# Performance work log

Measured on AMD Instinct MI355X. Metric: run time of the kernel, lower is better.

The kernel has to match this reference:

```python
import jax, jax.numpy as jnp
import numpy as np

B, S, E, H, L, F = 64, 256, 480, 6, 8, 1920
D = E // H  # 80
VOCAB, MEL, CHORD = 4833, 257, 4833 - 257
EPS = 1e-5


def setup_inputs() -> dict:
    key = jax.random.key(0)
    ks = jax.random.split(key, 24)
    mel = jax.random.randint(ks[0], (B, S), 0, MEL)
    chd = MEL + jax.random.randint(ks[1], (B, S), 0, CHORD)
    pos = jnp.arange(S) % 2  # 0=melody, 1=chord
    input_tokens = jnp.where(pos[None, :] == 1, chd, mel)
    std = 0.02
    n = lambda k, shp: std * jax.random.normal(k, shp, dtype=jnp.float32)
    return {
        'input_tokens': input_tokens,
        'tok_emb': n(ks[2], (VOCAB, E)),
        'pos_emb': n(ks[3], (S, E)),
        'Wq': n(ks[4], (L, E, E)), 'bq': jnp.zeros((L, E)),
        'Wk': n(ks[5], (L, E, E)), 'bk': jnp.zeros((L, E)),
        'Wv': n(ks[6], (L, E, E)), 'bv': jnp.zeros((L, E)),
        'Wo': n(ks[7], (L, E, E)), 'bo': jnp.zeros((L, E)),
        'ln1_s': jnp.ones((L, E)), 'ln1_b': jnp.zeros((L, E)),
        'ln2_s': jnp.ones((L, E)), 'ln2_b': jnp.zeros((L, E)),
        'W1': n(ks[8], (L, F, E)), 'b1': jnp.zeros((L, F)),
        'W2': n(ks[9], (L, E, F)), 'b2': jnp.zeros((L, E)),
        'Wh': n(ks[10], (CHORD, E)), 'bh': jnp.zeros((CHORD,)),
    }


def _ln(x, s, b):
    mu = jnp.mean(x, -1, keepdims=True)
    var = jnp.var(x, -1, keepdims=True)
    return (x - mu) * jax.lax.rsqrt(var + EPS) * s + b


def reference(input_tokens, tok_emb, pos_emb, Wq, bq, Wk, bk, Wv, bv, Wo, bo,
              ln1_s, ln1_b, ln2_s, ln2_b, W1, b1, W2, b2, Wh, bh):
    x = tok_emb[input_tokens] + pos_emb[None, :, :]  # [B,S,E]
    causal = jnp.tril(jnp.ones((S, S), dtype=bool))  # True = keep
    scale = 1.0 / jnp.sqrt(jnp.float32(D))
    for i in range(L):
        h = _ln(x, ln1_s[i], ln1_b[i])
        q = (h @ Wq[i].T + bq[i]).reshape(B, S, H, D).transpose(0, 2, 1, 3)
        k = (h @ Wk[i].T + bk[i]).reshape(B, S, H, D).transpose(0, 2, 1, 3)
        v = (h @ Wv[i].T + bv[i]).reshape(B, S, H, D).transpose(0, 2, 1, 3)
        scores = jnp.einsum('bhsd,bhtd->bhst', q, k) * scale
        scores = jnp.where(causal[None, None], scores, -jnp.inf)
        attn = jax.nn.softmax(scores, axis=-1)
        o = jnp.einsum('bhst,bhtd->bhsd', attn, v)
        o = o.transpose(0, 2, 1, 3).reshape(B, S, E)
        x = x + (o @ Wo[i].T + bo[i])
        h2 = _ln(x, ln2_s[i], ln2_b[i])
        ff = jax.nn.gelu(h2 @ W1[i].T + b1[i], approximate=False) @ W2[i].T + b2[i]
        x = x + ff
    chord = x[:, 1::2, :]  # [B, S//2, E]
    return chord @ Wh.T + bh
```

## Files before the change

### kernel.cpp

```cpp
#include <hip/hip_runtime.h>
#include <hip/hip_bf16.h>
#include <math.h>

#define B_ 64
#define S_ 256
#define E_ 480
#define H_ 6
#define D_ 80
#define L_ 8
#define F_ 1920
#define CHORD_ 4576
#define TOKENS_ (B_*S_)
#define CROWS_ (B_*128)
#define QS_ 1440
#define KP_ 512

typedef unsigned short u16;
typedef unsigned int u32;
typedef unsigned long long u64;
typedef __attribute__((ext_vector_type(8))) short short8;
typedef __attribute__((ext_vector_type(4))) float f32x4;
typedef __attribute__((ext_vector_type(4))) u32 u32x4;

__device__ __forceinline__ u16 f2bf(float f){
  u32 u = __float_as_uint(f);
  return (u16)((u + 0x7fffu + ((u >> 16) & 1u)) >> 16);
}

__device__ __forceinline__ void async_cp16(void* lds, const void* g){
  __builtin_amdgcn_global_load_lds((const __attribute__((address_space(1))) void*)g,
                                   (__attribute__((address_space(3))) void*)lds, 16, 0, 0);
}

__device__ __forceinline__ void xcd_tile(int gx, int gy, int& tx, int& ty){
  const int nwg = gx * gy;
  const int bid = blockIdx.y * gx + blockIdx.x;
  const int xcd = bid & 7, slot = bid >> 3;
  const int q8 = nwg >> 3, r8 = nwg & 7;
  const int t = slot + (xcd < r8 ? xcd * (q8 + 1) : r8 * (q8 + 1) + (xcd - r8) * q8);
  ty = t / gx;
  tx = t - ty * gx;
}

__global__ void cvt_kernel(const float* __restrict__ s, u16* __restrict__ d, int n4)
{
  int i = blockIdx.x * 256 + threadIdx.x;
  const int stride = gridDim.x * 256;
  for (; i < n4; i += stride){
    float4 v = ((const float4*)s)[i];
    u64 w = (u64)((u32)f2bf(v.x) | ((u32)f2bf(v.y) << 16))
          | ((u64)((u32)f2bf(v.z) | ((u32)f2bf(v.w) << 16)) << 32);
    ((u64*)d)[i] = w;
  }
}

__global__ void cvt_pad_kernel(const float* __restrict__ s, u16* __restrict__ d, int nrows)
{
  const int tot = nrows * 128;
  int i = blockIdx.x * 256 + threadIdx.x;
  const int stride = gridDim.x * 256;
  for (; i < tot; i += stride){
    int row = i >> 7, c4 = i & 127;
    u64 w = 0;
    if (c4 < 120){
      float4 v = ((const float4*)(s + (size_t)row * E_))[c4];
      w = (u64)((u32)f2bf(v.x) | ((u32)f2bf(v.y) << 16))
        | ((u64)((u32)f2bf(v.z) | ((u32)f2bf(v.w) << 16)) << 32);
    }
    ((u64*)d)[i] = w;
  }
}

__global__ void qkv_cvt_kernel(const float* __restrict__ Wq, const float* __restrict__ Wk,
                               const float* __restrict__ Wv, u16* __restrict__ dst)
{
  const int tot = L_ * QS_ * 128;
  int i = blockIdx.x * 256 + threadIdx.x;
  const int stride = gridDim.x * 256;
  for (; i < tot; i += stride){
    int l = i / (QS_*128);
    int rem = i - l*(QS_*128);
    int row = rem >> 7, c4 = rem & 127;
    u64 w = 0;
    if (c4 < 120){
      const float* src = (row < 480) ? Wq + (size_t)l*E_*E_ + (size_t)row*E_
                       : (row < 960) ? Wk + (size_t)l*E_*E_ + (size_t)(row-480)*E_
                                     : Wv + (size_t)l*E_*E_ + (size_t)(row-960)*E_;
      float4 v = ((const float4*)src)[c4];
      w = (u64)((u32)f2bf(v.x) | ((u32)f2bf(v.y) << 16))
        | ((u64)((u32)f2bf(v.z) | ((u32)f2bf(v.w) << 16)) << 32);
    }
    ((u64*)dst)[i] = w;
  }
}

__global__ void bias_cat_kernel(const float* __restrict__ bq, const float* __restrict__ bk,
                                const float* __restrict__ bv, float* __restrict__ dst)
{
  int i = blockIdx.x * 256 + threadIdx.x;
  if (i >= L_*QS_) return;
  int l = i / QS_, c = i - l*QS_;
  float v = (c < 480) ? bq[l*480 + c] : (c < 960) ? bk[l*480 + c - 480] : bv[l*480 + c - 960];
  dst[i] = v;
}

__global__ void embed_kernel(const int* __restrict__ tok,
                             const float* __restrict__ tok_emb,
                             const float* __restrict__ pos_emb,
                             float* __restrict__ x)
{
  int row = blockIdx.x;
  int s = row & (S_-1);
  int t = tok[row];
  const float* te = tok_emb + (size_t)t * E_;
  const float* pe = pos_emb + (size_t)s * E_;
  float* xr = x + (size_t)row * E_;
  for (int e = threadIdx.x; e < E_; e += blockDim.x)
    xr[e] = te[e] + pe[e];
}

__global__ __launch_bounds__(256) void ln_kernel(const float* __restrict__ x,
    const float* __restrict__ g, const float* __restrict__ b, u16* __restrict__ o,
    int ldo, int pad)
{
  int wid = threadIdx.x >> 6, lane = threadIdx.x & 63;
  int row = blockIdx.x * 4 + wid;
  const float* xr = x + (size_t)row * E_;
  float v[8];
  #pragma unroll
  for (int i = 0; i < 7; ++i) v[i] = xr[lane + i*64];
  v[7] = (lane < 32) ? xr[448 + lane] : 0.f;
  float sum = 0.f, sq = 0.f;
  #pragma unroll
  for (int i = 0; i < 8; ++i){ sum += v[i]; sq += v[i]*v[i]; }
  #pragma unroll
  for (int m = 1; m < 64; m <<= 1){ sum += __shfl_xor(sum, m); sq += __shfl_xor(sq, m); }
  float mean = sum * (1.f/E_);
  float var  = sq  * (1.f/E_) - mean*mean;
  float rs = rsqrtf(var + 1e-5f);
  u16* orow = o + (size_t)row * ldo;
  #pragma unroll
  for (int i = 0; i < 7; ++i){
    int idx = lane + i*64;
    orow[idx] = f2bf((v[i]-mean)*rs*g[idx] + b[idx]);
  }
  if (lane < 32){
    int idx = 448 + lane;
    orow[idx] = f2bf((v[7]-mean)*rs*g[idx] + b[idx]);
  }
  if (pad && lane < 32) orow[480 + lane] = 0;
}

template<int MODE>
__global__ __launch_bounds__(512) void gemm_tall_kernel(const u16* __restrict__ A,
                            const u16* __restrict__ Wb, const float* __restrict__ bias,
                            u16* __restrict__ Cb, float* __restrict__ Cf,
                            int M, int N, int K, int ldc)
{
  __shared__ u16 As[2][256*32];
  __shared__ u16 Ws[2][128*32];
  const int tid = threadIdx.x;
  const int wid = tid >> 6, lane = tid & 63;
  const int wm = wid >> 1, wn = wid & 1;
  const int lr = lane & 15, kg = lane >> 4;
  const int kgs = kg ^ (lr & 3);
  int tx, ty;
  xcd_tile(gridDim.x, gridDim.y, tx, ty);
  const int m0 = ty * 256;
  const int n0 = tx * 128;

  const f32x4 zero = {0.f,0.f,0.f,0.f};
  f32x4 acc[4][4];
  #pragma unroll
  for (int i=0;i<4;i++)
    #pragma unroll
    for (int j=0;j<4;j++)
      acc[i][j] = zero;

  const int srow = tid >> 2;
  const int schunk = (tid & 3) ^ (srow & 3);
  const u16* ap0 = A + (size_t)(m0 + srow) * K + schunk*8;
  const u16* ap1 = ap0 + (size_t)128 * K;
  int r0 = n0 + srow;
  if (r0 >= N) r0 = N-1;
  const u16* wp0 = Wb + (size_t)r0 * K + schunk*8;

  #define STAGE(bb, k0) do { \
    char* ab = (char*)As[bb] + wid*1024; \
    char* wb_ = (char*)Ws[bb] + wid*1024; \
    async_cp16(ab,        ap0 + (k0)); \
    async_cp16(ab + 8192, ap1 + (k0)); \
    async_cp16(wb_,        wp0 + (k0)); \
  } while(0)

  const int nsteps = K >> 5;
  STAGE(0, 0);
  __syncthreads();
  int cur = 0;
  for (int ks = 0; ks < nsteps; ++ks){
    if (ks + 1 < nsteps) STAGE(cur^1, (ks+1) << 5);

    short8 af[4], wf[4];
    #pragma unroll
    for (int i=0;i<4;i++) af[i] = *(const short8*)&As[cur][(wm*64 + i*16 + lr)*32 + kgs*8];
    #pragma unroll
    for (int j=0;j<4;j++) wf[j] = *(const short8*)&Ws[cur][(wn*64 + j*16 + lr)*32 + kgs*8];
    #pragma unroll
    for (int i=0;i<4;i++)
      #pragma unroll
      for (int j=0;j<4;j++)
        acc[i][j] = __builtin_amdgcn_mfma_f32_16x16x32_bf16(af[i], wf[j], acc[i][j], 0, 0, 0);

    __syncthreads();
    cur ^= 1;
  }
  #undef STAGE

  #pragma unroll
  for (int i=0;i<4;i++){
    const int row = m0 + wm*64 + i*16 + kg*4;
    #pragma unroll
    for (int j=0;j<4;j++){
      const int col = n0 + wn*64 + j*16 + lr;
      if (col < N){
        const float bv = bias[col];
        #pragma unroll
        for (int q=0;q<4;q++){
          float val = acc[i][j][q] + bv;
          size_t off = (size_t)(row + q) * ldc + col;
          if (MODE == 0){
            Cb[off] = f2bf(val);
          } else if (MODE == 1){
            float gx = 0.5f * val * (1.f + erff(val * 0.70710678118654752f));
            Cb[off] = f2bf(gx);
          } else if (MODE == 2){
            Cf[off] += val;
          } else {
            Cf[off] = val;
          }
        }
      }
    }
  }
}

template<int MODE>
__global__ __launch_bounds__(256, 4) void gemm_bf_kernel(const u16* __restrict__ A,
                            const u16* __restrict__ Wb, const float* __restrict__ bias,
                            u16* __restrict__ Cb, float* __restrict__ Cf,
                            int M, int N, int K, int ldc)
{
  __shared__ u16 As[2][128*32];
  __shared__ u16 Ws[2][128*32];
  const int tid = threadIdx.x;
  const int wid = tid >> 6, lane = tid & 63;
  const int wr = wid >> 1, wc = wid & 1;
  const int lr = lane & 15, kg = lane >> 4;
  const int kgs = kg ^ (lr & 3);
  int tx, ty;
  xcd_tile(gridDim.x, gridDim.y, tx, ty);
  const int m0 = ty * 128;
  const int n0 = tx * 128;

  const f32x4 zero = {0.f,0.f,0.f,0.f};
  f32x4 acc[4][4];
  #pragma unroll
  for (int i=0;i<4;i++)
    #pragma unroll
    for (int j=0;j<4;j++)
      acc[i][j] = zero;

  const int srow = tid >> 2;
  const int schunk = (tid & 3) ^ (srow & 3);
  const u16* ap0 = A + (size_t)(m0 + srow) * K + schunk*8;
  const u16* ap1 = ap0 + (size_t)64 * K;
  int r0 = n0 + srow, r1 = r0 + 64;
  if (r0 >= N) r0 = N-1;
  if (r1 >= N) r1 = N-1;
  const u16* wp0 = Wb + (size_t)r0 * K + schunk*8;
  const u16* wp1 = Wb + (size_t)r1 * K + schunk*8;

  #define STAGE(bb, k0) do { \
    char* ab = (char*)As[bb] + wid*1024; \
    char* wb_ = (char*)Ws[bb] + wid*1024; \
    async_cp16(ab,        ap0 + (k0)); \
    async_cp16(ab + 4096, ap1 + (k0)); \
    async_cp16(wb_,        wp0 + (k0)); \
    async_cp16(wb_ + 4096, wp1 + (k0)); \
  } while(0)

  const int nsteps = K >> 5;
  STAGE(0, 0);
  __syncthreads();
  int cur = 0;
  for (int ks = 0; ks < nsteps; ++ks){
    if (ks + 1 < nsteps) STAGE(cur^1, (ks+1) << 5);

    short8 af[4], wf[4];
    #pragma unroll
    for (int i=0;i<4;i++) af[i] = *(const short8*)&As[cur][(wr*64 + i*16 + lr)*32 + kgs*8];
    #pragma unroll
    for (int j=0;j<4;j++) wf[j] = *(const short8*)&Ws[cur][(wc*64 + j*16 + lr)*32 + kgs*8];
    #pragma unroll
    for (int i=0;i<4;i++)
      #pragma unroll
      for (int j=0;j<4;j++)
        acc[i][j] = __builtin_amdgcn_mfma_f32_16x16x32_bf16(af[i], wf[j], acc[i][j], 0, 0, 0);

    __syncthreads();
    cur ^= 1;
  }
  #undef STAGE

  #pragma unroll
  for (int i=0;i<4;i++){
    const int row = m0 + wr*64 + i*16 + kg*4;
    #pragma unroll
    for (int j=0;j<4;j++){
      const int col = n0 + wc*64 + j*16 + lr;
      if (col < N){
        const float bv = bias[col];
        #pragma unroll
        for (int q=0;q<4;q++){
          float val = acc[i][j][q] + bv;
          size_t off = (size_t)(row + q) * ldc + col;
          if (MODE == 0){
            Cb[off] = f2bf(val);
          } else if (MODE == 1){
            float gx = 0.5f * val * (1.f + erff(val * 0.70710678118654752f));
            Cb[off] = f2bf(gx);
          } else if (MODE == 2){
            Cf[off] += val;
          } else {
            Cf[off] = val;
          }
        }
      }
    }
  }
}

template<int MODE>
__global__ __launch_bounds__(256) void gemm_kernel(const u16* __restrict__ A, const float* __restrict__ W,
                            const float* __restrict__ bias,
                            u16* __restrict__ Cb, float* __restrict__ Cf,
                            int M, int N, int K, int ldc)
{
  __shared__ u16 As[128*32];
  __shared__ u16 Ws[128*32];
  const int tid = threadIdx.x;
  const int wid = tid >> 6, lane = tid & 63;
  const int wr = wid >> 1, wc = wid & 1;
  const int lr = lane & 15, kg = lane >> 4;
  int tx, ty;
  xcd_tile(gridDim.x, gridDim.y, tx, ty);
  const int m0 = ty * 128;
  const int n0 = tx * 128;

  const f32x4 zero = {0.f,0.f,0.f,0.f};
  f32x4 acc[4][4];
  #pragma unroll
  for (int i=0;i<4;i++)
    #pragma unroll
    for (int j=0;j<4;j++)
      acc[i][j] = zero;

  const int trow = tid >> 1;
  const int tcol = (tid & 1) * 16;
  const int wn = n0 + trow;
  const bool wok = wn < N;
  const float* wp = W + (size_t)wn * K + tcol;

  const u16* ap0 = A + (size_t)(m0 + (tid>>2)) * K + (tid&3)*8;
  const u16* ap1 = ap0 + (size_t)64 * K;
  char* lb0 = (char*)As + wid*1024;
  char* lb1 = (char*)As + 4096 + wid*1024;
  u32* wdst = (u32*)&Ws[trow*32 + tcol];

  const int nsteps = K >> 5;
  for (int ks = 0; ks < nsteps; ++ks){
    const int k0 = ks << 5;
    async_cp16(lb0, ap0 + k0);
    async_cp16(lb1, ap1 + k0);

    float wv[16];
    if (wok){
      const float4* s4 = (const float4*)(wp + k0);
      #pragma unroll
      for (int i=0;i<4;i++){
        float4 t4 = s4[i];
        wv[4*i]=t4.x; wv[4*i+1]=t4.y; wv[4*i+2]=t4.z; wv[4*i+3]=t4.w;
      }
    } else {
      #pragma unroll
      for (int i=0;i<16;i++) wv[i]=0.f;
    }
    u32 pk[8];
    #pragma unroll
    for (int i=0;i<8;i++) pk[i] = (u32)f2bf(wv[2*i]) | ((u32)f2bf(wv[2*i+1]) << 16);
    #pragma unroll
    for (int i=0;i<8;i++) wdst[i] = pk[i];

    __syncthreads();

    short8 af[4], wf[4];
    #pragma unroll
    for (int i=0;i<4;i++) af[i] = *(const short8*)&As[(wr*64 + i*16 + lr)*32 + kg*8];
    #pragma unroll
    for (int j=0;j<4;j++) wf[j] = *(const short8*)&Ws[(wc*64 + j*16 + lr)*32 + kg*8];
    #pragma unroll
    for (int i=0;i<4;i++)
      #pragma unroll
      for (int j=0;j<4;j++)
        acc[i][j] = __builtin_amdgcn_mfma_f32_16x16x32_bf16(af[i], wf[j], acc[i][j], 0, 0, 0);

    __syncthreads();
  }

  #pragma unroll
  for (int i=0;i<4;i++){
    const int row = m0 + wr*64 + i*16 + kg*4;
    #pragma unroll
    for (int j=0;j<4;j++){
      const int col = n0 + wc*64 + j*16 + lr;
      if (col < N){
        const float bv = bias[col];
        #pragma unroll
        for (int q=0;q<4;q++){
          float val = acc[i][j][q] + bv;
          size_t off = (size_t)(row + q) * ldc + col;
          if (MODE == 0){
            Cb[off] = f2bf(val);
          } else if (MODE == 1){
            float gx = 0.5f * val * (1.f + erff(val * 0.70710678118654752f));
            Cb[off] = f2bf(gx);
          } else if (MODE == 2){
            Cf[off] += val;
          } else {
            Cf[off] = val;
          }
        }
      }
    }
  }
}

#define KSTRIDE 104
#define VSTRIDE 264
__global__ __launch_bounds__(256) void attn_mfma_kernel(const u16* __restrict__ QKV,
                                                        u16* __restrict__ O)
{
  __shared__ u16 ks[256*KSTRIDE];
  __shared__ u16 vt[80*VSTRIDE];
  const int bh = blockIdx.x;
  const int b = bh / H_, h = bh - b*H_;
  const int tid = threadIdx.x;
  const int wv = tid >> 6, lane = tid & 63;
  const int q16 = lane & 15, g = lane >> 4;
  const size_t rowbase = (size_t)(b*S_ + tid) * QS_ + h * D_;

  {
    const uint4* kr = (const uint4*)(QKV + rowbase + 480);
    uint4 t0[10];
    #pragma unroll
    for (int i=0;i<10;i++) t0[i] = kr[i];
    u16* krow = &ks[tid*KSTRIDE];
    #pragma unroll
    for (int i=0;i<10;i++) *(uint4*)&krow[i*8] = t0[i];
    const uint4 z4 = {0,0,0,0};
    *(uint4*)&krow[80] = z4;
    *(uint4*)&krow[88] = z4;
  }
  {
    const u32* vr = (const u32*)(QKV + rowbase + 960);
    u32 t1[40];
    #pragma unroll
    for (int i=0;i<40;i++) t1[i] = vr[i];
    #pragma unroll
    for (int i=0;i<40;i++){
      vt[(2*i)*VSTRIDE + tid]   = (u16)(t1[i] & 0xffffu);
      vt[(2*i+1)*VSTRIDE + tid] = (u16)(t1[i] >> 16);
    }
  }
  short8 bq[4][3];
  const short8 z8 = {0,0,0,0,0,0,0,0};
  #pragma unroll
  for (int i=0;i<4;i++){
    const int qr = 16*wv + 64*i;
    const u16* qrow = QKV + (size_t)(b*S_ + qr + q16) * QS_ + h*D_;
    bq[i][0] = *(const short8*)&qrow[g*8];
    bq[i][1] = *(const short8*)&qrow[32 + g*8];
    bq[i][2] = (g < 2) ? *(const short8*)&qrow[64 + g*8] : z8;
  }
  __syncthreads();

  f32x4 o_[4][5];
  float m_[4], l_[4];
  #pragma unroll
  for (int i=0;i<4;i++){
    m_[i] = -1e30f; l_[i] = 0.f;
    #pragma unroll
    for (int j=0;j<5;j++) o_[i][j] = (f32x4){0.f,0.f,0.f,0.f};
  }
  const float scale = 0.1118033988749895f;
  const int ktmaxw = (16*wv + 207) >> 5;

  for (int kt = 0; kt <= ktmaxw; ++kt){
    short8 af[2][3];
    #pragma unroll
    for (int a=0;a<2;a++)
      #pragma unroll
      for (int kk=0;kk<3;kk++)
        af[a][kk] = *(const short8*)&ks[(32*kt + 16*a + q16)*KSTRIDE + kk*32 + g*8];
    short8 bvv[5];
    #pragma unroll
    for (int j=0;j<5;j++)
      bvv[j] = *(const short8*)&vt[(16*j + q16)*VSTRIDE + kt*32 + g*8];

    #pragma unroll
    for (int i=0;i<4;i++){
      const int qr = 16*wv + 64*i;
      if (kt > ((qr + 15) >> 5)) continue;
      f32x4 c0 = {0.f,0.f,0.f,0.f}, c1 = {0.f,0.f,0.f,0.f};
      #pragma unroll
      for (int kk=0;kk<3;kk++){
        c0 = __builtin_amdgcn_mfma_f32_16x16x32_bf16(af[0][kk], bq[i][kk], c0, 0, 0, 0);
        c1 = __builtin_amdgcn_mfma_f32_16x16x32_bf16(af[1][kk], bq[i][kk], c1, 0, 0, 0);
      }
      const int qglob = qr + q16;
      const int kb0 = 32*kt + 4*g;
      const bool diag = (32*kt + 31) > qr;
      float s0[4], s1[4];
      #pragma unroll
      for (int r=0;r<4;r++){
        s0[r] = c0[r] * scale;
        s1[r] = c1[r] * scale;
        if (diag){
          if (kb0 + r > qglob)      s0[r] = -3e38f;
          if (kb0 + 16 + r > qglob) s1[r] = -3e38f;
        }
      }
      float mx = fmaxf(fmaxf(fmaxf(s0[0],s0[1]),fmaxf(s0[2],s0[3])),
                       fmaxf(fmaxf(s1[0],s1[1]),fmaxf(s1[2],s1[3])));
      mx = fmaxf(mx, __shfl_xor(mx, 16));
      mx = fmaxf(mx, __shfl_xor(mx, 32));
      const float mnew = fmaxf(m_[i], mx);
      const float resc = __expf(m_[i] - mnew);
      float p0[4], p1[4], ps = 0.f;
      #pragma unroll
      for (int r=0;r<4;r++){
        p0[r] = __expf(s0[r] - mnew);
        p1[r] = __expf(s1[r] - mnew);
        ps += p0[r] + p1[r];
      }
      ps += __shfl_xor(ps, 16);
      ps += __shfl_xor(ps, 32);
      l_[i] = l_[i] * resc + ps;
      m_[i] = mnew;
      float fr[4];
      #pragma unroll
      for (int r=0;r<4;r++) fr[r] = __shfl(resc, 4*g + r);
      #pragma unroll
      for (int j=0;j<5;j++){
        #pragma unroll
        for (int r=0;r<4;r++) o_[i][j][r] *= fr[r];
      }
      u32 pw0 = (u32)f2bf(p0[0]) | ((u32)f2bf(p0[1]) << 16);
      u32 pw1 = (u32)f2bf(p0[2]) | ((u32)f2bf(p0[3]) << 16);
      u32 pw2 = (u32)f2bf(p1[0]) | ((u32)f2bf(p1[1]) << 16);
      u32 pw3 = (u32)f2bf(p1[2]) | ((u32)f2bf(p1[3]) << 16);
      const int s01 = ((((g<<1)&3)<<4) + q16) << 2;
      const int s23 = (((((g<<1)+1)&3)<<4) + q16) << 2;
      int rA0 = __builtin_amdgcn_ds_bpermute(s01, (int)pw0);
      int rB0 = __builtin_amdgcn_ds_bpermute(s01, (int)pw2);
      int rA1 = __builtin_amdgcn_ds_bpermute(s01, (int)pw1);
      int rB1 = __builtin_amdgcn_ds_bpermute(s01, (int)pw3);
      int rA2 = __builtin_amdgcn_ds_bpermute(s23, (int)pw0);
      int rB2 = __builtin_amdgcn_ds_bpermute(s23, (int)pw2);
      int rA3 = __builtin_amdgcn_ds_bpermute(s23, (int)pw1);
      int rB3 = __builtin_amdgcn_ds_bpermute(s23, (int)pw3);
      const bool lo = (g < 2);
      u32x4 rw = { (u32)(lo ? rA0 : rB0), (u32)(lo ? rA1 : rB1),
                   (u32)(lo ? rA2 : rB2), (u32)(lo ? rA3 : rB3) };
      short8 pa = __builtin_bit_cast(short8, rw);
      #pragma unroll
      for (int j=0;j<5;j++)
        o_[i][j] = __builtin_amdgcn_mfma_f32_16x16x32_bf16(pa, bvv[j], o_[i][j], 0, 0, 0);
    }
  }

  #pragma unroll
  for (int i=0;i<4;i++){
    const int qr = 16*wv + 64*i;
    const float inv = 1.f / l_[i];
    float fr[4];
    #pragma unroll
    for (int r=0;r<4;r++) fr[r] = __shfl(inv, 4*g + r);
    #pragma unroll
    for (int j=0;j<5;j++){
      #pragma unroll
      for (int r=0;r<4;r++){
        const int row = qr + 4*g + r;
        O[(size_t)(b*S_ + row) * E_ + h*D_ + 16*j + q16] = f2bf(o_[i][j][r] * fr[r]);
      }
    }
  }
}

__global__ void gather_kernel(const float* __restrict__ x, u16* __restrict__ cin, int ld)
{
  int i = blockIdx.x * 256 + threadIdx.x;
  if (i >= CROWS_*ld) return;
  int row = i / ld, col = i - row*ld;
  int b = row >> 7, r = row & 127;
  cin[i] = (col < E_) ? f2bf(x[((size_t)(b*S_ + 2*r + 1))*E_ + col]) : (u16)0;
}

extern "C" void kernel_launch(void* const* d_in, const int* in_sizes, int n_in,
                              void* d_out, int out_size, void* d_ws, size_t ws_size,
                              hipStream_t stream)
{
  (void)in_sizes; (void)n_in; (void)out_size;
  const int*   tok     = (const int*)d_in[0];
  const float* tok_emb = (const float*)d_in[1];
  const float* pos_emb = (const float*)d_in[2];
  const float* Wq = (const float*)d_in[3];
  const float* bq = (const float*)d_in[4];
  const float* Wk = (const float*)d_in[5];
  const float* bk = (const float*)d_in[6];
  const float* Wv = (const float*)d_in[7];
  const float* bv = (const float*)d_in[8];
  const float* Wo = (const float*)d_in[9];
  const float* bo = (const float*)d_in[10];
  const float* ln1s = (const float*)d_in[11];
  const float* ln1b = (const float*)d_in[12];
  const float* ln2s = (const float*)d_in[13];
  const float* ln2b = (const float*)d_in[14];
  const float* W1 = (const float*)d_in[15];
  const float* b1 = (const float*)d_in[16];
  const float* W2 = (const float*)d_in[17];
  const float* b2 = (const float*)d_in[18];
  const float* Wh = (const float*)d_in[19];
  const float* bh = (const float*)d_in[20];

  char* p = (char*)d_ws;
  float* x  = (float*)p;            p += (size_t)TOKENS_*E_*4;
  u16* h    = (u16*)p;              p += (size_t)TOKENS_*KP_*2;
  u16* qkv  = (u16*)p;
  u16* ao   = qkv + (size_t)TOKENS_*QS_;
  u16* ff1  = qkv;
  u16* cin  = h;
  p += (size_t)TOKENS_*QS_*2 + (size_t)TOKENS_*E_*2;

  const size_t szE  = (size_t)L_*E_*E_;
  u16* wqkv_bf = (u16*)p;            p += (size_t)L_*QS_*KP_*2;
  u16* wo_bf   = (u16*)p;            p += szE*2;
  u16* w1_bf   = (u16*)p;            p += (size_t)L_*F_*KP_*2;
  u16* w2_bf   = (u16*)p;            p += (size_t)L_*E_*F_*2;
  u16* wh_bf   = (u16*)p;            p += (size_t)CHORD_*KP_*2;
  float* bqkv  = (float*)p;          p += (size_t)L_*QS_*4;
  const size_t need = (size_t)(p - (char*)d_ws);
  const bool bf16w = (ws_size >= need);

  embed_kernel<<<TOKENS_, 128, 0, stream>>>(tok, tok_emb, pos_emb, x);

  dim3 blk(256);
  dim3 blk512(512);

  if (bf16w){
    qkv_cvt_kernel<<<2048, blk, 0, stream>>>(Wq, Wk, Wv, wqkv_bf);
    bias_cat_kernel<<<(L_*QS_ + 255)/256, blk, 0, stream>>>(bq, bk, bv, bqkv);
    cvt_kernel<<<1024, blk, 0, stream>>>(Wo, wo_bf, (int)(szE/4));
    cvt_pad_kernel<<<2048, blk, 0, stream>>>(W1, w1_bf, L_*F_);
    cvt_kernel<<<1024, blk, 0, stream>>>(W2, w2_bf, (int)((size_t)L_*E_*F_/4));
    cvt_pad_kernel<<<1024, blk, 0, stream>>>(Wh, wh_bf, CHORD_);
    for (int i = 0; i < L_; ++i){
      ln_kernel<<<TOKENS_/4, blk, 0, stream>>>(x, ln1s + i*E_, ln1b + i*E_, h, KP_, 1);
      gemm_tall_kernel<0><<<dim3(12, 64), blk512, 0, stream>>>(h, wqkv_bf + (size_t)i*QS_*KP_, bqkv + i*QS_, qkv, nullptr, TOKENS_, QS_, KP_, QS_);
      attn_mfma_kernel<<<B_*H_, blk, 0, stream>>>(qkv, ao);
      gemm_bf_kernel<2><<<dim3(4, 128), blk, 0, stream>>>(ao, wo_bf + (size_t)i*E_*E_, bo + i*E_, nullptr, x, TOKENS_, E_, E_, E_);
      ln_kernel<<<TOKENS_/4, blk, 0, stream>>>(x, ln2s + i*E_, ln2b + i*E_, h, KP_, 1);
      gemm_tall_kernel<1><<<dim3(15, 64), blk512, 0, stream>>>(h, w1_bf + (size_t)i*F_*KP_, b1 + i*F_, ff1, nullptr, TOKENS_, F_, KP_, F_);
      gemm_tall_kernel<2><<<dim3(4, 64), blk512, 0, stream>>>(ff1, w2_bf + (size_t)i*E_*F_, b2 + i*E_, nullptr, x, TOKENS_, E_, F_, E_);
    }
    gather_kernel<<<(CROWS_*KP_ + 255)/256, blk, 0, stream>>>(x, cin, KP_);
    gemm_tall_kernel<3><<<dim3(36, 32), blk512, 0, stream>>>(cin, wh_bf, bh, nullptr, (float*)d_out, CROWS_, CHORD_, KP_, CHORD_);
  } else {
    for (int i = 0; i < L_; ++i){
      ln_kernel<<<TOKENS_/4, blk, 0, stream>>>(x, ln1s + i*E_, ln1b + i*E_, h, E_, 0);
      gemm_kernel<0><<<dim3(4, 128), blk, 0, stream>>>(h, Wq + (size_t)i*E_*E_, bq + i*E_, qkv, nullptr, TOKENS_, E_, E_, QS_);
      gemm_kernel<0><<<dim3(4, 128), blk, 0, stream>>>(h, Wk + (size_t)i*E_*E_, bk + i*E_, qkv + 480, nullptr, TOKENS_, E_, E_, QS_);
      gemm_kernel<0><<<dim3(4, 128), blk, 0, stream>>>(h, Wv + (size_t)i*E_*E_, bv + i*E_, qkv + 960, nullptr, TOKENS_, E_, E_, QS_);
      attn_mfma_kernel<<<B_*H_, blk, 0, stream>>>(qkv, ao);
      gemm_kernel<2><<<dim3(4, 128), blk, 0, stream>>>(ao, Wo + (size_t)i*E_*E_, bo + i*E_, nullptr, x, TOKENS_, E_, E_, E_);
      ln_kernel<<<TOKENS_/4, blk, 0, stream>>>(x, ln2s + i*E_, ln2b + i*E_, h, E_, 0);
      gemm_kernel<1><<<dim3(15, 128), blk, 0, stream>>>(h, W1 + (size_t)i*F_*E_, b1 + i*F_, ff1, nullptr, TOKENS_, F_, E_, F_);
      gemm_kernel<2><<<dim3(4, 128), blk, 0, stream>>>(ff1, W2 + (size_t)i*E_*F_, b2 + i*E_, nullptr, x, TOKENS_, E_, F_, E_);
    }
    gather_kernel<<<(CROWS_*E_ + 255)/256, blk, 0, stream>>>(x, cin, E_);
    gemm_kernel<3><<<dim3(36, 64), blk, 0, stream>>>(cin, Wh, bh, nullptr, (float*)d_out, CROWS_, CHORD_, E_, CHORD_);
  }
}
```

Before: 2.155 ms.

## Triple-buffer GEMM LDS staging with explicit vmcnt waits and split barriers

Both bf16 GEMM kernels move from double- to triple-buffered async global-to-LDS staging, prefetching two K-steps ahead. The full __syncthreads is replaced by explicit s_waitcnt vmcnt/lgkmcnt waits plus raw s_barrier, so loads for later stages stay in flight during compute. MFMA sections are also wrapped in s_setprio. This costs 50% more LDS per block, which may lower occupancy. It also relies on hand-counted vmcnt values matching the number of async copies per stage.

Result: slower. 2.198 ms (+2.0%).

```diff
diff --git a/kernel.cpp b/kernel.cpp
--- a/kernel.cpp
+++ b/kernel.cpp
@@ -21,6 +21,9 @@
 typedef __attribute__((ext_vector_type(8))) short short8;
 typedef __attribute__((ext_vector_type(4))) float f32x4;
 typedef __attribute__((ext_vector_type(4))) u32 u32x4;
+
+#define VMCNT(n) asm volatile("s_waitcnt vmcnt(" #n ")" ::: "memory")
+#define LGKMCNT0 asm volatile("s_waitcnt lgkmcnt(0)" ::: "memory")
 
 __device__ __forceinline__ u16 f2bf(float f){
   u32 u = __float_as_uint(f);
@@ -157,8 +160,8 @@
                             u16* __restrict__ Cb, float* __restrict__ Cf,
                             int M, int N, int K, int ldc)
 {
-  __shared__ u16 As[2][256*32];
-  __shared__ u16 Ws[2][128*32];
+  __shared__ u16 As[3*256*32];
+  __shared__ u16 Ws[3*128*32];
   const int tid = threadIdx.x;
   const int wid = tid >> 6, lane = tid & 63;
   const int wm = wid >> 1, wn = wid & 1;
@@ -186,8 +189,8 @@
   const u16* wp0 = Wb + (size_t)r0 * K + schunk*8;
 
   #define STAGE(bb, k0) do { \
-    char* ab = (char*)As[bb] + wid*1024; \
-    char* wb_ = (char*)Ws[bb] + wid*1024; \
+    char* ab = (char*)As + (bb)*16384 + wid*1024; \
+    char* wb_ = (char*)Ws + (bb)*8192 + wid*1024; \
     async_cp16(ab,        ap0 + (k0)); \
     async_cp16(ab + 8192, ap1 + (k0)); \
     async_cp16(wb_,        wp0 + (k0)); \
@@ -195,24 +198,34 @@
 
   const int nsteps = K >> 5;
   STAGE(0, 0);
-  __syncthreads();
+  if (nsteps > 1) STAGE(1, 32);
   int cur = 0;
   for (int ks = 0; ks < nsteps; ++ks){
-    if (ks + 1 < nsteps) STAGE(cur^1, (ks+1) << 5);
+    const int nxt = (cur == 2) ? 0 : cur + 1;
+    const int nxt2 = (nxt == 2) ? 0 : nxt + 1;
+    if (ks + 2 < nsteps) STAGE(nxt2, (ks+2) << 5);
+
+    if (ks + 2 < nsteps)      VMCNT(6);
+    else if (ks + 1 < nsteps) VMCNT(3);
+    else                      VMCNT(0);
+    __builtin_amdgcn_s_barrier();
 
     short8 af[4], wf[4];
     #pragma unroll
-    for (int i=0;i<4;i++) af[i] = *(const short8*)&As[cur][(wm*64 + i*16 + lr)*32 + kgs*8];
-    #pragma unroll
-    for (int j=0;j<4;j++) wf[j] = *(const short8*)&Ws[cur][(wn*64 + j*16 + lr)*32 + kgs*8];
+    for (int i=0;i<4;i++) af[i] = *(const short8*)&As[cur*8192 + (wm*64 + i*16 + lr)*32 + kgs*8];
+    #pragma unroll
+    for (int j=0;j<4;j++) wf[j] = *(const short8*)&Ws[cur*4096 + (wn*64 + j*16 + lr)*32 + kgs*8];
+    LGKMCNT0;
+    __builtin_amdgcn_s_barrier();
+
+    __builtin_amdgcn_s_setprio(1);
     #pragma unroll
     for (int i=0;i<4;i++)
       #pragma unroll
       for (int j=0;j<4;j++)
         acc[i][j] = __builtin_amdgcn_mfma_f32_16x16x32_bf16(af[i], wf[j], acc[i][j], 0, 0, 0);
-
-    __syncthreads();
-    cur ^= 1;
+    __builtin_amdgcn_s_setprio(0);
+    cur = nxt;
   }
   #undef STAGE
 
@@ -250,8 +263,8 @@
                             u16* __restrict__ Cb, float* __restrict__ Cf,
                             int M, int N, int K, int ldc)
 {
-  __shared__ u16 As[2][128*32];
-  __shared__ u16 Ws[2][128*32];
+  __shared__ u16 As[3*128*32];
+  __shared__ u16 Ws[3*128*32];
   const int tid = threadIdx.x;
   const int wid = tid >> 6, lane = tid & 63;
   const int wr = wid >> 1, wc = wid & 1;
@@ -281,8 +294,8 @@
   const u16* wp1 = Wb + (size_t)r1 * K + schunk*8;
 
   #define STAGE(bb, k0) do { \
-    char* ab = (char*)As[bb] + wid*1024; \
-    char* wb_ = (char*)Ws[bb] + wid*1024; \
+    char* ab = (char*)As + (bb)*8192 + wid*1024; \
+    char* wb_ = (char*)Ws + (bb)*8192 + wid*1024; \
     async_cp16(ab,        ap0 + (k0)); \
     async_cp16(ab + 4096, ap1 + (k0)); \
     async_cp16(wb_,        wp0 + (k0)); \
@@ -291,24 +304,34 @@
 
   const int nsteps = K >> 5;
   STAGE(0, 0);
-  __syncthreads();
+  if (nsteps > 1) STAGE(1, 32);
   int cur = 0;
   for (int ks = 0; ks < nsteps; ++ks){
-    if (ks + 1 < nsteps) STAGE(cur^1, (ks+1) << 5);
+    const int nxt = (cur == 2) ? 0 : cur + 1;
+    const int nxt2 = (nxt == 2) ? 0 : nxt + 1;
+    if (ks + 2 < nsteps) STAGE(nxt2, (ks+2) << 5);
+
+    if (ks + 2 < nsteps)      VMCNT(8);
+    else if (ks + 1 < nsteps) VMCNT(4);
+    else                      VMCNT(0);
+    __builtin_amdgcn_s_barrier();
 
     short8 af[4], wf[4];
     #pragma unroll
-    for (int i=0;i<4;i++) af[i] = *(const short8*)&As[cur][(wr*64 + i*16 + lr)*32 + kgs*8];
-    #pragma unroll
-    for (int j=0;j<4;j++) wf[j] = *(const short8*)&Ws[cur][(wc*64 + j*16 + lr)*32 + kgs*8];
+    for (int i=0;i<4;i++) af[i] = *(const short8*)&As[cur*4096 + (wr*64 + i*16 + lr)*32 + kgs*8];
+    #pragma unroll
+    for (int j=0;j<4;j++) wf[j] = *(const short8*)&Ws[cur*4096 + (wc*64 + j*16 + lr)*32 + kgs*8];
+    LGKMCNT0;
+    __builtin_amdgcn_s_barrier();
+
+    __builtin_amdgcn_s_setprio(1);
     #pragma unroll
     for (int i=0;i<4;i++)
       #pragma unroll
       for (int j=0;j<4;j++)
         acc[i][j] = __builtin_amdgcn_mfma_f32_16x16x32_bf16(af[i], wf[j], acc[i][j], 0, 0, 0);
-
-    __syncthreads();
-    cur ^= 1;
+    __builtin_amdgcn_s_setprio(0);
+    cur = nxt;
   }
   #undef STAGE
 
```

## Fuse FFN up-projection, GELU and down-projection into one kernel

Applied to the files above, without the earlier changes.

Replaces the two FFN GEMMs with a single ffn_kernel. For each 64-row tile it computes 96-wide chunks of the hidden layer, applies bias and GELU into shared memory, and accumulates the second GEMM in registers. This avoids writing the 16384x1920 intermediate to global memory and reading it back. The kernel uses explicit waitcnt and barrier pipelining, but launches only 256 blocks and every block rereads all of W1 and W2. The tall 256-row GEMM is also dropped in favour of the 128x128 gemm_bf_kernel for the QKV and head projections.

Result: slower. 2.859 ms (+32.7%).

```diff
diff --git a/kernel.cpp b/kernel.cpp
--- a/kernel.cpp
+++ b/kernel.cpp
@@ -21,6 +21,9 @@
 typedef __attribute__((ext_vector_type(8))) short short8;
 typedef __attribute__((ext_vector_type(4))) float f32x4;
 typedef __attribute__((ext_vector_type(4))) u32 u32x4;
+
+#define VMCNT(n) asm volatile("s_waitcnt vmcnt(" #n ")" ::: "memory")
+#define LGKMCNT0 asm volatile("s_waitcnt lgkmcnt(0)" ::: "memory")
 
 __device__ __forceinline__ u16 f2bf(float f){
   u32 u = __float_as_uint(f);
@@ -152,99 +155,6 @@
 }
 
 template<int MODE>
-__global__ __launch_bounds__(512) void gemm_tall_kernel(const u16* __restrict__ A,
-                            const u16* __restrict__ Wb, const float* __restrict__ bias,
-                            u16* __restrict__ Cb, float* __restrict__ Cf,
-                            int M, int N, int K, int ldc)
-{
-  __shared__ u16 As[2][256*32];
-  __shared__ u16 Ws[2][128*32];
-  const int tid = threadIdx.x;
-  const int wid = tid >> 6, lane = tid & 63;
-  const int wm = wid >> 1, wn = wid & 1;
-  const int lr = lane & 15, kg = lane >> 4;
-  const int kgs = kg ^ (lr & 3);
-  int tx, ty;
-  xcd_tile(gridDim.x, gridDim.y, tx, ty);
-  const int m0 = ty * 256;
-  const int n0 = tx * 128;
-
-  const f32x4 zero = {0.f,0.f,0.f,0.f};
-  f32x4 acc[4][4];
-  #pragma unroll
-  for (int i=0;i<4;i++)
-    #pragma unroll
-    for (int j=0;j<4;j++)
-      acc[i][j] = zero;
-
-  const int srow = tid >> 2;
-  const int schunk = (tid & 3) ^ (srow & 3);
-  const u16* ap0 = A + (size_t)(m0 + srow) * K + schunk*8;
-  const u16* ap1 = ap0 + (size_t)128 * K;
-  int r0 = n0 + srow;
-  if (r0 >= N) r0 = N-1;
-  const u16* wp0 = Wb + (size_t)r0 * K + schunk*8;
-
-  #define STAGE(bb, k0) do { \
-    char* ab = (char*)As[bb] + wid*1024; \
-    char* wb_ = (char*)Ws[bb] + wid*1024; \
-    async_cp16(ab,        ap0 + (k0)); \
-    async_cp16(ab + 8192, ap1 + (k0)); \
-    async_cp16(wb_,        wp0 + (k0)); \
-  } while(0)
-
-  const int nsteps = K >> 5;
-  STAGE(0, 0);
-  __syncthreads();
-  int cur = 0;
-  for (int ks = 0; ks < nsteps; ++ks){
-    if (ks + 1 < nsteps) STAGE(cur^1, (ks+1) << 5);
-
-    short8 af[4], wf[4];
-    #pragma unroll
-    for (int i=0;i<4;i++) af[i] = *(const short8*)&As[cur][(wm*64 + i*16 + lr)*32 + kgs*8];
-    #pragma unroll
-    for (int j=0;j<4;j++) wf[j] = *(const short8*)&Ws[cur][(wn*64 + j*16 + lr)*32 + kgs*8];
-    #pragma unroll
-    for (int i=0;i<4;i++)
-      #pragma unroll
-      for (int j=0;j<4;j++)
-        acc[i][j] = __builtin_amdgcn_mfma_f32_16x16x32_bf16(af[i], wf[j], acc[i][j], 0, 0, 0);
-
-    __syncthreads();
-    cur ^= 1;
-  }
-  #undef STAGE
-
-  #pragma unroll
-  for (int i=0;i<4;i++){
-    const int row = m0 + wm*64 + i*16 + kg*4;
-    #pragma unroll
-    for (int j=0;j<4;j++){
-      const int col = n0 + wn*64 + j*16 + lr;
-      if (col < N){
-        const float bv = bias[col];
-        #pragma unroll
-        for (int q=0;q<4;q++){
-          float val = acc[i][j][q] + bv;
-          size_t off = (size_t)(row + q) * ldc + col;
-          if (MODE == 0){
-            Cb[off] = f2bf(val);
-          } else if (MODE == 1){
-            float gx = 0.5f * val * (1.f + erff(val * 0.70710678118654752f));
-            Cb[off] = f2bf(gx);
-          } else if (MODE == 2){
-            Cf[off] += val;
-          } else {
-            Cf[off] = val;
-          }
-        }
-      }
-    }
-  }
-}
-
-template<int MODE>
 __global__ __launch_bounds__(256, 4) void gemm_bf_kernel(const u16* __restrict__ A,
                             const u16* __restrict__ Wb, const float* __restrict__ bias,
                             u16* __restrict__ Cb, float* __restrict__ Cf,
@@ -326,9 +236,6 @@
           size_t off = (size_t)(row + q) * ldc + col;
           if (MODE == 0){
             Cb[off] = f2bf(val);
-          } else if (MODE == 1){
-            float gx = 0.5f * val * (1.f + erff(val * 0.70710678118654752f));
-            Cb[off] = f2bf(gx);
           } else if (MODE == 2){
             Cf[off] += val;
           } else {
@@ -338,6 +245,144 @@
       }
     }
   }
+}
+
+__global__ __launch_bounds__(384) void ffn_kernel(const u16* __restrict__ h,
+    const u16* __restrict__ W1b, const float* __restrict__ b1,
+    const u16* __restrict__ W2b, const float* __restrict__ b2,
+    float* __restrict__ x)
+{
+  __shared__ u16 hs[64*520];
+  __shared__ u16 w1s[3][96*32];
+  __shared__ u16 ps[64*104];
+  __shared__ u16 w2s[2][480*32];
+  const int tid = threadIdx.x;
+  const int wid = tid >> 6, lane = tid & 63;
+  const int lr = lane & 15, kg = lane >> 4;
+  const int kgs = kg ^ (lr & 3);
+  const int g4 = kg * 4;
+  const int r0 = blockIdx.x * 64;
+  const int wa_r = wid / 3, wa_c = wid - wa_r*3;
+  const int srow = tid >> 2;
+  const int sw = (tid & 3) ^ (srow & 3);
+
+  for (int r = wid; r < 64; r += 6)
+    async_cp16(&hs[r*520], &h[(size_t)(r0 + r)*KP_ + lane*8]);
+
+  #define STAGE_W1(slot, f0q, ksq) \
+    async_cp16((char*)w1s[slot] + wid*1024, &W1b[(size_t)((f0q) + srow)*E_ + (ksq)*32 + sw*8])
+  #define STAGE_W2(buf, f0q, kkq) do { \
+    _Pragma("unroll") \
+    for (int ii = 0; ii < 5; ++ii) \
+      async_cp16((char*)w2s[buf] + ii*6144 + wid*1024, \
+                 &W2b[(size_t)(ii*96 + srow)*F_ + (f0q) + (kkq)*32 + sw*8]); \
+  } while(0)
+
+  const f32x4 zero = {0.f,0.f,0.f,0.f};
+  f32x4 acc2[4][5];
+  #pragma unroll
+  for (int i=0;i<4;i++)
+    #pragma unroll
+    for (int j=0;j<5;j++)
+      acc2[i][j] = zero;
+
+  STAGE_W1(0, 0, 0);
+  STAGE_W1(1, 0, 1);
+
+  for (int c = 0; c < 20; ++c){
+    const int f0 = c * 96;
+    f32x4 acc1[2][2];
+    #pragma unroll
+    for (int i=0;i<2;i++)
+      #pragma unroll
+      for (int j=0;j<2;j++)
+        acc1[i][j] = zero;
+
+    for (int ks = 0; ks < 15; ++ks){
+      const int slot = ks % 3;
+      if (ks + 2 < 15) STAGE_W1((ks+2)%3, f0, ks+2);
+      if (ks + 2 < 15)      VMCNT(2);
+      else if (ks + 1 < 15) VMCNT(1);
+      else                  VMCNT(0);
+      __builtin_amdgcn_s_barrier();
+      short8 haf[2], wf[2];
+      haf[0] = *(const short8*)&hs[(wa_r*32 +      lr)*520 + ks*32 + kg*8];
+      haf[1] = *(const short8*)&hs[(wa_r*32 + 16 + lr)*520 + ks*32 + kg*8];
+      wf[0]  = *(const short8*)&w1s[slot][(wa_c*32 +      lr)*32 + kgs*8];
+      wf[1]  = *(const short8*)&w1s[slot][(wa_c*32 + 16 + lr)*32 + kgs*8];
+      LGKMCNT0;
+      __builtin_amdgcn_s_barrier();
+      acc1[0][0] = __builtin_amdgcn_mfma_f32_16x16x32_bf16(haf[0], wf[0], acc1[0][0], 0, 0, 0);
+      acc1[0][1] = __builtin_amdgcn_mfma_f32_16x16x32_bf16(haf[0], wf[1], acc1[0][1], 0, 0, 0);
+      acc1[1][0] = __builtin_amdgcn_mfma_f32_16x16x32_bf16(haf[1], wf[0], acc1[1][0], 0, 0, 0);
+      acc1[1][1] = __builtin_amdgcn_mfma_f32_16x16x32_bf16(haf[1], wf[1], acc1[1][1], 0, 0, 0);
+    }
+
+    STAGE_W2(0, f0, 0);
+
+    {
+      float b1v[2];
+      b1v[0] = b1[f0 + wa_c*32 +      lr];
+      b1v[1] = b1[f0 + wa_c*32 + 16 + lr];
+      #pragma unroll
+      for (int i=0;i<2;i++)
+        #pragma unroll
+        for (int j=0;j<2;j++)
+          #pragma unroll
+          for (int q=0;q<4;q++){
+            float v = acc1[i][j][q] + b1v[j];
+            float gx = 0.5f * v * (1.f + erff(v * 0.70710678118654752f));
+            ps[(wa_r*32 + i*16 + g4 + q)*104 + wa_c*32 + j*16 + lr] = f2bf(gx);
+          }
+    }
+    LGKMCNT0;
+    VMCNT(0);
+    __builtin_amdgcn_s_barrier();
+
+    for (int kk = 0; kk < 3; ++kk){
+      if (kk == 0){
+        STAGE_W2(1, f0, 1);
+      } else if (kk == 1){
+        STAGE_W2(0, f0, 2);
+        if (c + 1 < 20){ STAGE_W1(0, f0+96, 0); STAGE_W1(1, f0+96, 1); }
+        if (c + 1 < 20) VMCNT(7);
+        else            VMCNT(5);
+      } else {
+        if (c + 1 < 20) VMCNT(2);
+        else            VMCNT(0);
+      }
+      __builtin_amdgcn_s_barrier();
+      const int buf = kk & 1;
+      short8 af2[4], wf2[5];
+      #pragma unroll
+      for (int i=0;i<4;i++) af2[i] = *(const short8*)&ps[(i*16 + lr)*104 + kk*32 + kg*8];
+      #pragma unroll
+      for (int j=0;j<5;j++) wf2[j] = *(const short8*)&w2s[buf][(wid*80 + j*16 + lr)*32 + kgs*8];
+      LGKMCNT0;
+      __builtin_amdgcn_s_barrier();
+      #pragma unroll
+      for (int i=0;i<4;i++)
+        #pragma unroll
+        for (int j=0;j<5;j++)
+          acc2[i][j] = __builtin_amdgcn_mfma_f32_16x16x32_bf16(af2[i], wf2[j], acc2[i][j], 0, 0, 0);
+    }
+  }
+
+  #pragma unroll
+  for (int i=0;i<4;i++){
+    #pragma unroll
+    for (int j=0;j<5;j++){
+      const int col = wid*80 + j*16 + lr;
+      const float bv = b2[col];
+      #pragma unroll
+      for (int q=0;q<4;q++){
+        const int row = r0 + i*16 + g4 + q;
+        x[(size_t)row*E_ + col] += acc2[i][j][q] + bv;
+      }
+    }
+  }
+  #undef STAGE_W1
+  #undef STAGE_W2
 }
 
 template<int MODE>
@@ -648,14 +693,13 @@
   u16* h    = (u16*)p;              p += (size_t)TOKENS_*KP_*2;
   u16* qkv  = (u16*)p;
   u16* ao   = qkv + (size_t)TOKENS_*QS_;
-  u16* ff1  = qkv;
   u16* cin  = h;
   p += (size_t)TOKENS_*QS_*2 + (size_t)TOKENS_*E_*2;
 
   const size_t szE  = (size_t)L_*E_*E_;
   u16* wqkv_bf = (u16*)p;            p += (size_t)L_*QS_*KP_*2;
   u16* wo_bf   = (u16*)p;            p += szE*2;
-  u16* w1_bf   = (u16*)p;            p += (size_t)L_*F_*KP_*2;
+  u16* w1_bf   = (u16*)p;            p += (size_t)L_*F_*E_*2;
   u16* w2_bf   = (u16*)p;            p += (size_t)L_*E_*F_*2;
   u16* wh_bf   = (u16*)p;            p += (size_t)CHORD_*KP_*2;
   float* bqkv  = (float*)p;          p += (size_t)L_*QS_*4;
@@ -665,27 +709,27 @@
   embed_kernel<<<TOKENS_, 128, 0, stream>>>(tok, tok_emb, pos_emb, x);
 
   dim3 blk(256);
-  dim3 blk512(512);
 
   if (bf16w){
     qkv_cvt_kernel<<<2048, blk, 0, stream>>>(Wq, Wk, Wv, wqkv_bf);
     bias_cat_kernel<<<(L_*QS_ + 255)/256, blk, 0, stream>>>(bq, bk, bv, bqkv);
     cvt_kernel<<<1024, blk, 0, stream>>>(Wo, wo_bf, (int)(szE/4));
-    cvt_pad_kernel<<<2048, blk, 0, stream>>>(W1, w1_bf, L_*F_);
-    cvt_kernel<<<1024, blk, 0, stream>>>(W2, w2_bf, (int)((size_t)L_*E_*F_/4));
+    cvt_kernel<<<2048, blk, 0, stream>>>(W1, w1_bf, (int)((size_t)L_*F_*E_/4));
+    cvt_kernel<<<2048, blk, 0, stream>>>(W2, w2_bf, (int)((size_t)L_*E_*F_/4));
     cvt_pad_kernel<<<1024, blk, 0, stream>>>(Wh, wh_bf, CHORD_);
     for (int i = 0; i < L_; ++i){
       ln_kernel<<<TOKENS_/4, blk, 0, stream>>>(x, ln1s + i*E_, ln1b + i*E_, h, KP_, 1);
-      gemm_tall_kernel<0><<<dim3(12, 64), blk512, 0, stream>>>(h, wqkv_bf + (size_t)i*QS_*KP_, bqkv + i*QS_, qkv, nullptr, TOKENS_, QS_, KP_, QS_);
+      gemm_bf_kernel<0><<<dim3(12, 128), blk, 0, stream>>>(h, wqkv_bf + (size_t)i*QS_*KP_, bqkv + i*QS_, qkv, nullptr, TOKENS_, QS_, KP_, QS_);
       attn_mfma_kernel<<<B_*H_, blk, 0, stream>>>(qkv, ao);
       gemm_bf_kernel<2><<<dim3(4, 128), blk, 0, stream>>>(ao, wo_bf + (size_t)i*E_*E_, bo + i*E_, nullptr, x, TOKENS_, E_, E_, E_);
       ln_kernel<<<TOKENS_/4, blk, 0, stream>>>(x, ln2s + i*E_, ln2b + i*E_, h, KP_, 1);
-      gemm_tall_kernel<1><<<dim3(15, 64), blk512, 0, stream>>>(h, w1_bf + (size_t)i*F_*KP_, b1 + i*F_, ff1, nullptr, TOKENS_, F_, KP_, F_);
-      gemm_tall_kernel<2><<<dim3(4, 64), blk512, 0, stream>>>(ff1, w2_bf + (size_t)i*E_*F_, b2 + i*E_, nullptr, x, TOKENS_, E_, F_, E_);
+      ffn_kernel<<<TOKENS_/64, dim3(384), 0, stream>>>(h, w1_bf + (size_t)i*F_*E_, b1 + i*F_,
+                                                       w2_bf + (size_t)i*E_*F_, b2 + i*E_, x);
     }
     gather_kernel<<<(CROWS_*KP_ + 255)/256, blk, 0, stream>>>(x, cin, KP_);
-    gemm_tall_kernel<3><<<dim3(36, 32), blk512, 0, stream>>>(cin, wh_bf, bh, nullptr, (float*)d_out, CROWS_, CHORD_, KP_, CHORD_);
+    gemm_bf_kernel<3><<<dim3(36, 64), blk, 0, stream>>>(cin, wh_bf, bh, nullptr, (float*)d_out, CROWS_, CHORD_, KP_, CHORD_);
   } else {
+    u16* ff1 = qkv;
     for (int i = 0; i < L_; ++i){
       ln_kernel<<<TOKENS_/4, blk, 0, stream>>>(x, ln1s + i*E_, ln1b + i*E_, h, E_, 0);
       gemm_kernel<0><<<dim3(4, 128), blk, 0, stream>>>(h, Wq + (size_t)i*E_*E_, bq + i*E_, qkv, nullptr, TOKENS_, E_, E_, QS_);
```
